# Optimization experiments

Hardware: AMD Instinct MI355X
Metric: run time of the kernel (lower is better)

Reference implementation:

```python
import jax, jax.numpy as jnp
import numpy as np

B, S, H = 1, 2048, 2048
E, I = 16, 1408
I_SHARED = 5632
TOP_K = 2


def setup_inputs() -> dict:
    key = jax.random.key(0)
    ks = jax.random.split(key, 8)
    scale = 0.02
    return {
        "hidden_states": jax.random.normal(ks[0], (B, S, H), dtype=jnp.float32),
        "router_w": jax.random.normal(ks[1], (H, E), dtype=jnp.float32) * scale,
        "expert_gate_up_w": jax.random.normal(ks[2], (E, H, 2 * I), dtype=jnp.float32) * scale,
        "expert_out_w": jax.random.normal(ks[3], (E, I, H), dtype=jnp.float32) * scale,
        "shared_ffw_gate_w": jax.random.normal(ks[4], (H, I_SHARED), dtype=jnp.float32) * scale,
        "shared_ffw_inter_w": jax.random.normal(ks[5], (H, I_SHARED), dtype=jnp.float32) * scale,
        "shared_ffw_out_w": jax.random.normal(ks[6], (I_SHARED, H), dtype=jnp.float32) * scale,
        "shared_gate_w": jax.random.normal(ks[7], (H, 1), dtype=jnp.float32) * scale,
        "top_k": TOP_K,
    }


def reference(hidden_states, router_w, expert_gate_up_w, expert_out_w,
              shared_ffw_gate_w, shared_ffw_inter_w, shared_ffw_out_w,
              shared_gate_w, top_k):
    b, s, h = hidden_states.shape
    e = router_w.shape[-1]
    x = hidden_states.reshape(-1, h)  # [T, H]

    # --- Router: softmax over experts, top-k, renormalize (norm_top_k_prob=True) ---
    router_logits = x @ router_w                        # [T, E]
    router_probs = jax.nn.softmax(router_logits, -1)
    top_p, top_i = jax.lax.top_k(router_probs, top_k)   # [T, K]
    top_p = top_p / jnp.sum(top_p, axis=-1, keepdims=True)
    # dense routing matrix [E, T] (matches one_hot-sum-transpose in source)
    one_hot = jax.nn.one_hot(top_i, e, dtype=top_p.dtype)  # [T, K, E]
    routing_full = jnp.sum(one_hot * top_p[..., None], axis=1).T  # [E, T]

    # --- Dense per-expert SwiGLU over ALL tokens (as in QwenMoeExperts) ---
    gate_up = jnp.einsum('th,ehm->etm', x, expert_gate_up_w)  # [E, T, 2I]
    gate, up = jnp.split(gate_up, 2, axis=-1)
    hidden = up * jax.nn.silu(gate)                           # [E, T, I]
    expert_out = jnp.einsum('eti,eih->eth', hidden, expert_out_w)  # [E, T, H]
    expert_contribution = jnp.einsum('eth,et->th', expert_out, routing_full)

    # --- Shared expert (SwiGLU MLP) with sigmoid gate ---
    sgate = jax.nn.silu(x @ shared_ffw_gate_w)
    sinter = x @ shared_ffw_inter_w
    shared_out = (sinter * sgate) @ shared_ffw_out_w          # [T, H]
    shared_out = shared_out * jax.nn.sigmoid(x @ shared_gate_w)

    out = (expert_contribution + shared_out).reshape(b, s, h)
    return out, router_logits
```

## Files before the change

kernel.cpp:

```cpp
#include <hip/hip_runtime.h>
#include <math.h>

typedef __attribute__((ext_vector_type(4))) float f32x4;
typedef __attribute__((ext_vector_type(4))) unsigned int u32x4;
typedef __attribute__((ext_vector_type(8))) unsigned short u16x8;
typedef __attribute__((ext_vector_type(8))) __bf16 bf16x8;
typedef unsigned short ushort_t;

#define H_DIM 2048
#define T_TOK 2048
#define NEXP 16
#define I_DIM 1408
#define I2_DIM 2816
#define IS_DIM 5632
#define MAXROWS 8192

static __device__ __forceinline__ unsigned short f2bf(float f){
  union { float f; unsigned u; } v; v.f = f;
  unsigned r = v.u + 0x7FFFu + ((v.u >> 16) & 1u);
  return (unsigned short)(r >> 16);
}
static __device__ __forceinline__ float bf2f(unsigned short h){
  union { unsigned u; float f; } v; v.u = ((unsigned)h) << 16;
  return v.f;
}
static __device__ __forceinline__ float silu_f(float x){ return x / (1.f + __expf(-x)); }

static __device__ __forceinline__ void gld16(const ushort_t* g, ushort_t* l){
  __builtin_amdgcn_global_load_lds(
      (const __attribute__((address_space(1))) unsigned int*)g,
      (__attribute__((address_space(3))) unsigned int*)l, 16, 0, 0);
}

static __device__ __forceinline__ bf16x8 dsr128(unsigned byte_off){
  u32x4 r;
  asm volatile("ds_read_b128 %0, %1" : "=v"(r) : "v"(byte_off));
  return __builtin_bit_cast(bf16x8, r);
}

__global__ void cast_bf16_k(const float* __restrict__ in, ushort_t* __restrict__ out){
  long i = ((long)blockIdx.x * 256 + threadIdx.x) * 8;
  f32x4 a = *(const f32x4*)&in[i];
  f32x4 b = *(const f32x4*)&in[i + 4];
  union { ushort_t s[8]; u32x4 v; } pk;
  #pragma unroll
  for (int j = 0; j < 4; j++){ pk.s[j] = f2bf(a[j]); pk.s[j+4] = f2bf(b[j]); }
  *(u32x4*)&out[i] = pk.v;
}

__global__ void transpose_cast_k(const float* __restrict__ in, ushort_t* __restrict__ out,
                                 int K, int N){
  long zo = (long)blockIdx.z * K * N;
  in += zo; out += zo;
  __shared__ float tl[64][65];
  int n0 = blockIdx.x * 64, k0 = blockIdx.y * 64;
  int tid = threadIdx.x;
  int lr = tid >> 2;
  int lv = (tid & 3) * 4;
  #pragma unroll
  for (int j = 0; j < 4; j++){
    int col = lv + j * 16;
    f32x4 v = *(const f32x4*)&in[(long)(k0 + lr) * N + n0 + col];
    tl[lr][col + 0] = v[0]; tl[lr][col + 1] = v[1];
    tl[lr][col + 2] = v[2]; tl[lr][col + 3] = v[3];
  }
  __syncthreads();
  int nl = tid >> 3;
  int kc = (tid & 7) * 8;
  #pragma unroll
  for (int it = 0; it < 2; it++){
    int n = nl + it * 32;
    union { ushort_t s[8]; u32x4 v; } pk;
    #pragma unroll
    for (int j = 0; j < 8; j++) pk.s[j] = f2bf(tl[kc + j][n]);
    *(u32x4*)&out[(long)(n0 + n) * K + k0 + kc] = pk.v;
  }
}

__global__ void router_k(const float* __restrict__ x, const float* __restrict__ rw,
                         const float* __restrict__ sgw, float* __restrict__ logits,
                         int* __restrict__ counts, int* __restrict__ lists,
                         float* __restrict__ probs, float* __restrict__ sgmul){
  int wid = threadIdx.x >> 6, lane = threadIdx.x & 63;
  int t = blockIdx.x * 4 + wid;
  const float* xr = x + (long)t * H_DIM;
  float acc[17];
  #pragma unroll
  for (int e = 0; e < 17; e++) acc[e] = 0.f;
  for (int h0 = lane * 4; h0 < H_DIM; h0 += 256){
    f32x4 xv = *(const f32x4*)&xr[h0];
    #pragma unroll
    for (int i = 0; i < 4; i++){
      float xs = xv[i];
      const float* wrow = rw + (long)(h0 + i) * NEXP;
      #pragma unroll
      for (int e = 0; e < 16; e++) acc[e] += xs * wrow[e];
      acc[16] += xs * sgw[h0 + i];
    }
  }
  #pragma unroll
  for (int e = 0; e < 17; e++)
    for (int off = 32; off >= 1; off >>= 1)
      acc[e] += __shfl_xor(acc[e], off);
  if (lane == 0){
    float* lo = logits + (long)t * NEXP;
    #pragma unroll
    for (int e = 0; e < 16; e++) lo[e] = acc[e];
    int e0 = 0;
    #pragma unroll
    for (int e = 1; e < 16; e++) if (acc[e] > acc[e0]) e0 = e;
    int e1 = (e0 == 0) ? 1 : 0;
    #pragma unroll
    for (int e = 0; e < 16; e++) if (e != e0 && acc[e] > acc[e1]) e1 = e;
    float d = acc[e1] - acc[e0];
    float ed = __expf(d);
    float p0 = 1.f / (1.f + ed);
    float p1 = ed / (1.f + ed);
    int pos0 = atomicAdd(&counts[e0], 1);
    lists[e0 * T_TOK + pos0] = t; probs[e0 * T_TOK + pos0] = p0;
    int pos1 = atomicAdd(&counts[e1], 1);
    lists[e1 * T_TOK + pos1] = t; probs[e1 * T_TOK + pos1] = p1;
    sgmul[t] = 1.f / (1.f + __expf(-acc[16]));
  }
}

__global__ void bases_k(const int* __restrict__ counts, int* __restrict__ bases){
  if (threadIdx.x == 0){
    int r = 0;
    for (int e = 0; e < NEXP; e++){ bases[e] = r; r += (counts[e] + 127) & ~127; }
  }
}

__global__ void swiglu_expert_k(const ushort_t* __restrict__ gu, ushort_t* __restrict__ hid){
  long qd = (long)blockIdx.x * 256 + threadIdx.x;
  long r = qd / (I_DIM / 8); int ic = (int)(qd % (I_DIM / 8)) * 8;
  const ushort_t* g = gu + r * I2_DIM + ic;
  u16x8 gv = *(const u16x8*)g;
  u16x8 uv = *(const u16x8*)(g + I_DIM);
  u16x8 ov;
  #pragma unroll
  for (int i = 0; i < 8; i++)
    ov[i] = f2bf(bf2f(uv[i]) * silu_f(bf2f(gv[i])));
  *(u16x8*)&hid[r * I_DIM + ic] = ov;
}

__global__ void swiglu_flat_k(ushort_t* __restrict__ sg, const ushort_t* __restrict__ si){
  long i = ((long)blockIdx.x * 256 + threadIdx.x) * 8;
  u16x8 g = *(const u16x8*)&sg[i];
  u16x8 s = *(const u16x8*)&si[i];
  u16x8 o;
  #pragma unroll
  for (int j = 0; j < 8; j++)
    o[j] = f2bf(bf2f(s[j]) * silu_f(bf2f(g[j])));
  *(u16x8*)&sg[i] = o;
}

template<int MODE>
static __device__ __forceinline__ void gemm3_body(
    const ushort_t* __restrict__ A, const ushort_t* __restrict__ Bt,
    const ushort_t* __restrict__ Bt2, ushort_t* __restrict__ Cb,
    int K, int lda, int ldbt, int ldc, int mb,
    const int* __restrict__ counts, const int* __restrict__ bases,
    const int* __restrict__ lists, const float* __restrict__ probs,
    const float* __restrict__ svec, float* __restrict__ outp, long bstride){
  int z = blockIdx.z;
  int cnt = T_TOK;
  const ushort_t* Ab = A;
  const ushort_t* Bb = Bt;
  long rbase = 0;
  if constexpr (MODE == 0){ if (z){ Bb = Bt2; Cb += (long)T_TOK * ldc; } }
  if constexpr (MODE == 1){ cnt = counts[z]; rbase = bases[z]; Bb += (long)z * bstride; }
  if constexpr (MODE == 2){ cnt = counts[z]; Ab += (long)bases[z] * lda; Bb += (long)z * bstride; }

  int kb = K / gridDim.y;
  int kbase = blockIdx.y * kb;
  Ab += kbase;
  Bb += kbase;

  int nwg = gridDim.x;
  int wgo = blockIdx.x;
  int q = nwg >> 3, r = nwg & 7;
  int xcd = wgo & 7, idx = wgo >> 3;
  int wg = (xcd < r ? xcd * (q + 1) : r * (q + 1) + (xcd - r) * q) + idx;
  int m0 = (wg % mb) * 128;
  if (m0 >= cnt) return;
  int n0 = (wg / mb) * 128;

  __shared__ ushort_t lds[3 * 8192];
  unsigned lbase = (unsigned)(size_t)(__attribute__((address_space(3))) ushort_t*)lds;

  int tid = threadIdx.x;
  int lane = tid & 63;
  int wv = tid >> 6;
  int wm = wv >> 1;
  int wn = wv & 1;

  int srow = lane >> 2;
  int sslot = ((lane & 3) ^ (srow & 3)) * 8;
  long aoff[2], boff[2];
  #pragma unroll
  for (int c = 0; c < 2; c++){
    int mr = wv * 32 + c * 16 + srow;
    int grow;
    if constexpr (MODE == 1){
      int j = m0 + mr; if (j >= cnt) j = cnt - 1;
      grow = lists[z * T_TOK + j];
    } else {
      grow = m0 + mr;
    }
    aoff[c] = (long)grow * lda + sslot;
    boff[c] = (long)(n0 + mr) * ldbt + sslot;
  }

  auto stage = [&](int t, int buf){
    long ko = (long)t * 32;
    ushort_t* dA = lds + buf * 8192 + wv * 32 * 32;
    ushort_t* dB = dA + 4096;
    gld16(Ab + aoff[0] + ko, dA);
    gld16(Ab + aoff[1] + ko, dA + 512);
    gld16(Bb + boff[0] + ko, dB);
    gld16(Bb + boff[1] + ko, dB + 512);
  };

  f32x4 zero = {0.f, 0.f, 0.f, 0.f};
  f32x4 acc[4][4];
  #pragma unroll
  for (int i = 0; i < 4; i++)
    #pragma unroll
    for (int j = 0; j < 4; j++) acc[i][j] = zero;

  int fr = lane & 15;
  int kg = lane >> 4;
  unsigned ps = (unsigned)((kg ^ (fr & 3)) << 4);
  unsigned aoffb = (unsigned)((wm * 64 + fr) * 64) + ps;
  unsigned boffb = 8192u + (unsigned)((wn * 64 + fr) * 64) + ps;

  int nt = kb >> 5;
  stage(0, 0);
  __builtin_amdgcn_sched_barrier(0);
  stage(1, 1);

  int rb = 0, sb = 2;
  for (int t = 0; t < nt; t++){
    if (t + 2 < nt) asm volatile("s_waitcnt vmcnt(4)" ::: "memory");
    else            asm volatile("s_waitcnt vmcnt(0)" ::: "memory");
    __builtin_amdgcn_s_barrier();
    __builtin_amdgcn_sched_barrier(0);
    unsigned bufb = lbase + (unsigned)rb * 16384u;
    bf16x8 af[4], bg[4];
    #pragma unroll
    for (int f = 0; f < 4; f++){
      af[f] = dsr128(bufb + aoffb + f * 1024u);
      bg[f] = dsr128(bufb + boffb + f * 1024u);
    }
    __builtin_amdgcn_sched_barrier(0);
    if (t + 2 < nt) stage(t + 2, sb);
    asm volatile("s_waitcnt lgkmcnt(0)" ::: "memory");
    __builtin_amdgcn_sched_barrier(0);
    __builtin_amdgcn_s_setprio(1);
    #pragma unroll
    for (int fm = 0; fm < 4; fm++)
      #pragma unroll
      for (int fn = 0; fn < 4; fn++)
        acc[fm][fn] = __builtin_amdgcn_mfma_f32_16x16x32_bf16(af[fm], bg[fn], acc[fm][fn], 0, 0, 0);
    __builtin_amdgcn_s_setprio(0);
    rb = (rb == 2) ? 0 : rb + 1;
    sb = (sb == 2) ? 0 : sb + 1;
  }

  int colb = n0 + wn * 64 + (lane & 15);
  int rowb = m0 + wm * 64 + (lane >> 4) * 4;
  #pragma unroll
  for (int fm = 0; fm < 4; fm++){
    #pragma unroll
    for (int fn = 0; fn < 4; fn++){
      f32x4 v = acc[fm][fn];
      int col = colb + fn * 16;
      #pragma unroll
      for (int rr = 0; rr < 4; rr++){
        int m = rowb + fm * 16 + rr;
        if constexpr (MODE == 0){
          Cb[(long)m * ldc + col] = f2bf(v[rr]);
        } else if constexpr (MODE == 1){
          if (m < cnt) Cb[(rbase + m) * (long)ldc + col] = f2bf(v[rr]);
        } else if constexpr (MODE == 2){
          if (m < cnt){
            int tok = lists[z * T_TOK + m];
            float pp = probs[z * T_TOK + m];
            atomicAdd(outp + (long)tok * ldc + col, pp * v[rr]);
          }
        } else {
          atomicAdd(outp + (long)m * ldc + col, svec[m] * v[rr]);
        }
      }
    }
  }
}

#define GEMM_ARGS const ushort_t* A, const ushort_t* Bt, const ushort_t* Bt2, ushort_t* Cb, \
    int K, int lda, int ldbt, int ldc, int mb, const int* counts, const int* bases, \
    const int* lists, const float* probs, const float* svec, float* outp, long bstride
#define GEMM_PASS A, Bt, Bt2, Cb, K, lda, ldbt, ldc, mb, counts, bases, lists, probs, svec, outp, bstride

__global__ __launch_bounds__(256) void g_shared_gi(GEMM_ARGS){ gemm3_body<0>(GEMM_PASS); }
__global__ __launch_bounds__(256) void g_shared_out(GEMM_ARGS){ gemm3_body<3>(GEMM_PASS); }
__global__ __launch_bounds__(256) void g_expert_gu(GEMM_ARGS){ gemm3_body<1>(GEMM_PASS); }
__global__ __launch_bounds__(256) void g_expert_out(GEMM_ARGS){ gemm3_body<2>(GEMM_PASS); }

extern "C" void kernel_launch(void* const* d_in, const int* in_sizes, int n_in,
                              void* d_out, int out_size, void* d_ws, size_t ws_size,
                              hipStream_t stream){
  const float* x    = (const float*)d_in[0];
  const float* rw   = (const float*)d_in[1];
  const float* wgu  = (const float*)d_in[2];
  const float* wout = (const float*)d_in[3];
  const float* wsg  = (const float*)d_in[4];
  const float* wsi  = (const float*)d_in[5];
  const float* wso  = (const float*)d_in[6];
  const float* sgw  = (const float*)d_in[7];

  float* out = (float*)d_out;
  float* logits = out + (size_t)T_TOK * H_DIM;

  char* w = (char*)d_ws;
  auto alloc = [&](size_t b){ char* p = w; w += (b + 255) & ~(size_t)255; return p; };
  ushort_t* xb     = (ushort_t*)alloc((size_t)T_TOK * H_DIM * 2);
  ushort_t* wgu_t  = (ushort_t*)alloc((size_t)NEXP * I2_DIM * H_DIM * 2);
  ushort_t* wout_t = (ushort_t*)alloc((size_t)NEXP * H_DIM * I_DIM * 2);
  ushort_t* wsg_t  = (ushort_t*)alloc((size_t)IS_DIM * H_DIM * 2);
  ushort_t* wsi_t  = (ushort_t*)alloc((size_t)IS_DIM * H_DIM * 2);
  ushort_t* wso_t  = (ushort_t*)alloc((size_t)H_DIM * IS_DIM * 2);
  ushort_t* sgr    = (ushort_t*)alloc((size_t)2 * T_TOK * IS_DIM * 2);
  ushort_t* sir    = sgr + (size_t)T_TOK * IS_DIM;
  ushort_t* gu     = (ushort_t*)alloc((size_t)MAXROWS * I2_DIM * 2);
  ushort_t* hid    = (ushort_t*)alloc((size_t)MAXROWS * I_DIM * 2);
  int*   counts = (int*)alloc(64);
  int*   bases  = (int*)alloc(64);
  int*   lists  = (int*)alloc((size_t)NEXP * T_TOK * 4);
  float* probs  = (float*)alloc((size_t)NEXP * T_TOK * 4);
  float* sgmul  = (float*)alloc((size_t)T_TOK * 4);

  hipMemsetAsync(counts, 0, 64, stream);
  hipMemsetAsync(out, 0, (size_t)T_TOK * H_DIM * sizeof(float), stream);

  cast_bf16_k<<<2048, 256, 0, stream>>>(x, xb);
  transpose_cast_k<<<dim3(I2_DIM/64, H_DIM/64, NEXP), 256, 0, stream>>>(wgu, wgu_t, H_DIM, I2_DIM);
  transpose_cast_k<<<dim3(H_DIM/64, I_DIM/64, NEXP), 256, 0, stream>>>(wout, wout_t, I_DIM, H_DIM);
  transpose_cast_k<<<dim3(IS_DIM/64, H_DIM/64, 1), 256, 0, stream>>>(wsg, wsg_t, H_DIM, IS_DIM);
  transpose_cast_k<<<dim3(IS_DIM/64, H_DIM/64, 1), 256, 0, stream>>>(wsi, wsi_t, H_DIM, IS_DIM);
  transpose_cast_k<<<dim3(H_DIM/64, IS_DIM/64, 1), 256, 0, stream>>>(wso, wso_t, IS_DIM, H_DIM);

  router_k<<<512, 256, 0, stream>>>(x, rw, sgw, logits, counts, lists, probs, sgmul);
  bases_k<<<1, 64, 0, stream>>>(counts, bases);

  g_shared_gi<<<dim3((T_TOK/128) * (IS_DIM/128), 1, 2), 256, 0, stream>>>(
      xb, wsg_t, wsi_t, sgr, H_DIM, H_DIM, H_DIM, IS_DIM, T_TOK/128,
      nullptr, nullptr, nullptr, nullptr, nullptr, nullptr, 0);
  swiglu_flat_k<<<(T_TOK * (IS_DIM/8)) / 256, 256, 0, stream>>>(sgr, sir);
  g_shared_out<<<dim3((T_TOK/128) * (H_DIM/128), 4, 1), 256, 0, stream>>>(
      sgr, wso_t, nullptr, nullptr, IS_DIM, IS_DIM, IS_DIM, H_DIM, T_TOK/128,
      nullptr, nullptr, nullptr, nullptr, sgmul, out, 0);

  g_expert_gu<<<dim3((T_TOK/128) * (I2_DIM/128), 1, NEXP), 256, 0, stream>>>(
      xb, wgu_t, nullptr, gu, H_DIM, H_DIM, H_DIM, I2_DIM, T_TOK/128,
      counts, bases, lists, probs, nullptr, nullptr, (long)I2_DIM * H_DIM);
  swiglu_expert_k<<<((long)MAXROWS * (I_DIM/8)) / 256, 256, 0, stream>>>(gu, hid);
  g_expert_out<<<dim3((T_TOK/128) * (H_DIM/128), 1, NEXP), 256, 0, stream>>>(
      hid, wout_t, nullptr, nullptr, I_DIM, I_DIM, I_DIM, H_DIM, T_TOK/128,
      counts, bases, lists, probs, nullptr, out, (long)I_DIM * H_DIM);

  (void)in_sizes; (void)n_in; (void)out_size; (void)ws_size;
}
```

Before: 798.9 us.

## Enlarge GEMM tiles to 256x256 with 512 threads and double buffering

Switches all four GEMM kernels from 128x128 tiles with 256 threads and a three-stage LDS ring to 256x256 tiles with 512 threads (eight waves, each computing a 128x64 sub-tile) and a two-buffer ping-pong. Expert row bases are now padded to multiples of 256 to match the new M tile. The goal is more data reuse per LDS load and fewer redundant global reads of weights and activations. The cost is a shallower prefetch, since each iteration waits with vmcnt(0), plus higher register pressure from 128 accumulator registers per lane. It also brings coarser wave quantization and more wasted padding rows on experts whose token counts are not multiples of 256.

```diff
diff --git a/kernel.cpp b/kernel.cpp
--- a/kernel.cpp
+++ b/kernel.cpp
@@ -36,6 +36,9 @@
   u32x4 r;
   asm volatile("ds_read_b128 %0, %1" : "=v"(r) : "v"(byte_off));
   return __builtin_bit_cast(bf16x8, r);
+}
+static __device__ __forceinline__ unsigned ldsaddr(const ushort_t* p){
+  return (unsigned)(size_t)(const __attribute__((address_space(3))) ushort_t*)p;
 }
 
 __global__ void cast_bf16_k(const float* __restrict__ in, ushort_t* __restrict__ out){
@@ -127,7 +130,7 @@
 __global__ void bases_k(const int* __restrict__ counts, int* __restrict__ bases){
   if (threadIdx.x == 0){
     int r = 0;
-    for (int e = 0; e < NEXP; e++){ bases[e] = r; r += (counts[e] + 127) & ~127; }
+    for (int e = 0; e < NEXP; e++){ bases[e] = r; r += (counts[e] + 255) & ~255; }
   }
 }
 
@@ -156,7 +159,7 @@
 }
 
 template<int MODE>
-static __device__ __forceinline__ void gemm3_body(
+static __device__ __forceinline__ void gemm4_body(
     const ushort_t* __restrict__ A, const ushort_t* __restrict__ Bt,
     const ushort_t* __restrict__ Bt2, ushort_t* __restrict__ Cb,
     int K, int lda, int ldbt, int ldc, int mb,
@@ -182,18 +185,17 @@
   int q = nwg >> 3, r = nwg & 7;
   int xcd = wgo & 7, idx = wgo >> 3;
   int wg = (xcd < r ? xcd * (q + 1) : r * (q + 1) + (xcd - r) * q) + idx;
-  int m0 = (wg % mb) * 128;
+  int m0 = (wg % mb) * 256;
   if (m0 >= cnt) return;
-  int n0 = (wg / mb) * 128;
-
-  __shared__ ushort_t lds[3 * 8192];
-  unsigned lbase = (unsigned)(size_t)(__attribute__((address_space(3))) ushort_t*)lds;
+  int n0 = (wg / mb) * 256;
+
+  __shared__ ushort_t A0[8192], B0[8192], A1[8192], B1[8192];
 
   int tid = threadIdx.x;
   int lane = tid & 63;
   int wv = tid >> 6;
-  int wm = wv >> 1;
-  int wn = wv & 1;
+  int wm = wv >> 2;
+  int wn = wv & 3;
 
   int srow = lane >> 2;
   int sslot = ((lane & 3) ^ (srow & 3)) * 8;
@@ -212,66 +214,66 @@
     boff[c] = (long)(n0 + mr) * ldbt + sslot;
   }
 
-  auto stage = [&](int t, int buf){
-    long ko = (long)t * 32;
-    ushort_t* dA = lds + buf * 8192 + wv * 32 * 32;
-    ushort_t* dB = dA + 4096;
-    gld16(Ab + aoff[0] + ko, dA);
-    gld16(Ab + aoff[1] + ko, dA + 512);
-    gld16(Bb + boff[0] + ko, dB);
-    gld16(Bb + boff[1] + ko, dB + 512);
+  auto stg = [&](long t, ushort_t* dA, ushort_t* dB){
+    long ko = t * 32;
+    ushort_t* wA = dA + wv * 1024;
+    ushort_t* wB = dB + wv * 1024;
+    gld16(Ab + aoff[0] + ko, wA);
+    gld16(Ab + aoff[1] + ko, wA + 512);
+    gld16(Bb + boff[0] + ko, wB);
+    gld16(Bb + boff[1] + ko, wB + 512);
   };
 
   f32x4 zero = {0.f, 0.f, 0.f, 0.f};
-  f32x4 acc[4][4];
-  #pragma unroll
-  for (int i = 0; i < 4; i++)
+  f32x4 acc[8][4];
+  #pragma unroll
+  for (int i = 0; i < 8; i++)
     #pragma unroll
     for (int j = 0; j < 4; j++) acc[i][j] = zero;
 
-  int fr = lane & 15;
-  int kg = lane >> 4;
-  unsigned ps = (unsigned)((kg ^ (fr & 3)) << 4);
-  unsigned aoffb = (unsigned)((wm * 64 + fr) * 64) + ps;
-  unsigned boffb = 8192u + (unsigned)((wn * 64 + fr) * 64) + ps;
+  unsigned ps = (unsigned)(((lane >> 4) ^ (lane & 3)) << 4);
+  unsigned aro = (unsigned)((wm * 128 + (lane & 15)) * 64) + ps;
+  unsigned bro = (unsigned)((wn * 64 + (lane & 15)) * 64) + ps;
+  unsigned a0b = ldsaddr(A0), b0b = ldsaddr(B0);
+  unsigned a1b = ldsaddr(A1), b1b = ldsaddr(B1);
 
   int nt = kb >> 5;
-  stage(0, 0);
-  __builtin_amdgcn_sched_barrier(0);
-  stage(1, 1);
-
-  int rb = 0, sb = 2;
-  for (int t = 0; t < nt; t++){
-    if (t + 2 < nt) asm volatile("s_waitcnt vmcnt(4)" ::: "memory");
-    else            asm volatile("s_waitcnt vmcnt(0)" ::: "memory");
-    __builtin_amdgcn_s_barrier();
-    __builtin_amdgcn_sched_barrier(0);
-    unsigned bufb = lbase + (unsigned)rb * 16384u;
-    bf16x8 af[4], bg[4];
-    #pragma unroll
-    for (int f = 0; f < 4; f++){
-      af[f] = dsr128(bufb + aoffb + f * 1024u);
-      bg[f] = dsr128(bufb + boffb + f * 1024u);
-    }
-    __builtin_amdgcn_sched_barrier(0);
-    if (t + 2 < nt) stage(t + 2, sb);
-    asm volatile("s_waitcnt lgkmcnt(0)" ::: "memory");
-    __builtin_amdgcn_sched_barrier(0);
-    __builtin_amdgcn_s_setprio(1);
-    #pragma unroll
-    for (int fm = 0; fm < 4; fm++)
-      #pragma unroll
-      for (int fn = 0; fn < 4; fn++)
-        acc[fm][fn] = __builtin_amdgcn_mfma_f32_16x16x32_bf16(af[fm], bg[fn], acc[fm][fn], 0, 0, 0);
-    __builtin_amdgcn_s_setprio(0);
-    rb = (rb == 2) ? 0 : rb + 1;
-    sb = (sb == 2) ? 0 : sb + 1;
-  }
+  stg(0, A0, B0);
+
+  #define BODY(T, CURA, CURB, NXA, NXB)                                          \
+  {                                                                              \
+    asm volatile("s_waitcnt vmcnt(0)" ::: "memory");                             \
+    __builtin_amdgcn_s_barrier();                                                \
+    __builtin_amdgcn_sched_barrier(0);                                           \
+    if ((T) + 1 < nt) stg((T) + 1, NXA, NXB);                                    \
+    __builtin_amdgcn_sched_barrier(0);                                           \
+    bf16x8 af[8], bg[4];                                                         \
+    _Pragma("unroll")                                                            \
+    for (int f = 0; f < 8; f++) af[f] = dsr128(CURA + aro + f * 1024u);          \
+    _Pragma("unroll")                                                            \
+    for (int f = 0; f < 4; f++) bg[f] = dsr128(CURB + bro + f * 1024u);          \
+    asm volatile("s_waitcnt lgkmcnt(0)" ::: "memory");                           \
+    __builtin_amdgcn_sched_barrier(0);                                           \
+    __builtin_amdgcn_s_setprio(1);                                               \
+    _Pragma("unroll")                                                            \
+    for (int fm = 0; fm < 8; fm++)                                               \
+      _Pragma("unroll")                                                          \
+      for (int fn = 0; fn < 4; fn++)                                             \
+        acc[fm][fn] = __builtin_amdgcn_mfma_f32_16x16x32_bf16(af[fm], bg[fn],    \
+                                                              acc[fm][fn], 0, 0, 0); \
+    __builtin_amdgcn_s_setprio(0);                                               \
+  }
+
+  for (int t = 0; t < nt; t += 2){
+    BODY(t,     a0b, b0b, A1, B1);
+    BODY(t + 1, a1b, b1b, A0, B0);
+  }
+  #undef BODY
 
   int colb = n0 + wn * 64 + (lane & 15);
-  int rowb = m0 + wm * 64 + (lane >> 4) * 4;
-  #pragma unroll
-  for (int fm = 0; fm < 4; fm++){
+  int rowb = m0 + wm * 128 + (lane >> 4) * 4;
+  #pragma unroll
+  for (int fm = 0; fm < 8; fm++){
     #pragma unroll
     for (int fn = 0; fn < 4; fn++){
       f32x4 v = acc[fm][fn];
@@ -302,10 +304,10 @@
     const int* lists, const float* probs, const float* svec, float* outp, long bstride
 #define GEMM_PASS A, Bt, Bt2, Cb, K, lda, ldbt, ldc, mb, counts, bases, lists, probs, svec, outp, bstride
 
-__global__ __launch_bounds__(256) void g_shared_gi(GEMM_ARGS){ gemm3_body<0>(GEMM_PASS); }
-__global__ __launch_bounds__(256) void g_shared_out(GEMM_ARGS){ gemm3_body<3>(GEMM_PASS); }
-__global__ __launch_bounds__(256) void g_expert_gu(GEMM_ARGS){ gemm3_body<1>(GEMM_PASS); }
-__global__ __launch_bounds__(256) void g_expert_out(GEMM_ARGS){ gemm3_body<2>(GEMM_PASS); }
+__global__ __launch_bounds__(512) void g_shared_gi(GEMM_ARGS){ gemm4_body<0>(GEMM_PASS); }
+__global__ __launch_bounds__(512) void g_shared_out(GEMM_ARGS){ gemm4_body<3>(GEMM_PASS); }
+__global__ __launch_bounds__(512) void g_expert_gu(GEMM_ARGS){ gemm4_body<1>(GEMM_PASS); }
+__global__ __launch_bounds__(512) void g_expert_out(GEMM_ARGS){ gemm4_body<2>(GEMM_PASS); }
 
 extern "C" void kernel_launch(void* const* d_in, const int* in_sizes, int n_in,
                               void* d_out, int out_size, void* d_ws, size_t ws_size,
@@ -353,20 +355,20 @@
   router_k<<<512, 256, 0, stream>>>(x, rw, sgw, logits, counts, lists, probs, sgmul);
   bases_k<<<1, 64, 0, stream>>>(counts, bases);
 
-  g_shared_gi<<<dim3((T_TOK/128) * (IS_DIM/128), 1, 2), 256, 0, stream>>>(
-      xb, wsg_t, wsi_t, sgr, H_DIM, H_DIM, H_DIM, IS_DIM, T_TOK/128,
+  g_shared_gi<<<dim3((T_TOK/256) * (IS_DIM/256), 1, 2), 512, 0, stream>>>(
+      xb, wsg_t, wsi_t, sgr, H_DIM, H_DIM, H_DIM, IS_DIM, T_TOK/256,
       nullptr, nullptr, nullptr, nullptr, nullptr, nullptr, 0);
   swiglu_flat_k<<<(T_TOK * (IS_DIM/8)) / 256, 256, 0, stream>>>(sgr, sir);
-  g_shared_out<<<dim3((T_TOK/128) * (H_DIM/128), 4, 1), 256, 0, stream>>>(
-      sgr, wso_t, nullptr, nullptr, IS_DIM, IS_DIM, IS_DIM, H_DIM, T_TOK/128,
+  g_shared_out<<<dim3((T_TOK/256) * (H_DIM/256), 4, 1), 512, 0, stream>>>(
+      sgr, wso_t, nullptr, nullptr, IS_DIM, IS_DIM, IS_DIM, H_DIM, T_TOK/256,
       nullptr, nullptr, nullptr, nullptr, sgmul, out, 0);
 
-  g_expert_gu<<<dim3((T_TOK/128) * (I2_DIM/128), 1, NEXP), 256, 0, stream>>>(
-      xb, wgu_t, nullptr, gu, H_DIM, H_DIM, H_DIM, I2_DIM, T_TOK/128,
+  g_expert_gu<<<dim3((T_TOK/256) * (I2_DIM/256), 1, NEXP), 512, 0, stream>>>(
+      xb, wgu_t, nullptr, gu, H_DIM, H_DIM, H_DIM, I2_DIM, T_TOK/256,
       counts, bases, lists, probs, nullptr, nullptr, (long)I2_DIM * H_DIM);
   swiglu_expert_k<<<((long)MAXROWS * (I_DIM/8)) / 256, 256, 0, stream>>>(gu, hid);
-  g_expert_out<<<dim3((T_TOK/128) * (H_DIM/128), 1, NEXP), 256, 0, stream>>>(
-      hid, wout_t, nullptr, nullptr, I_DIM, I_DIM, I_DIM, H_DIM, T_TOK/128,
+  g_expert_out<<<dim3((T_TOK/256) * (H_DIM/256), 1, NEXP), 512, 0, stream>>>(
+      hid, wout_t, nullptr, nullptr, I_DIM, I_DIM, I_DIM, H_DIM, T_TOK/256,
       counts, bases, lists, probs, nullptr, out, (long)I_DIM * H_DIM);
 
   (void)in_sizes; (void)n_in; (void)out_size; (void)ws_size;
```

Measured after the change: 928.0 us. 16.2% more time.

## Merge shared and routed expert GEMMs into combined up and down launches

Applied to the files above, without the earlier changes.

Replaces four separate GEMM launches with two: one up-projection kernel covering the shared gate/inter and per-expert gate_up GEMMs, and one down-projection kernel covering the shared output (split-K of 2) and per-expert output GEMMs. Work is dispatched by blockIdx.z, and the template MODE becomes a runtime emode argument. The intent is to fill the GPU better by letting small, uneven expert tiles run alongside the large shared tiles, and to remove launch gaps and tail effects between kernels. MAXROWS is also reduced so the expert SwiGLU pass covers fewer rows. In exchange, the runtime branches in the epilogue may cost registers, and many early-exiting blocks in the expert z-slices still take a launch slot.

```diff
diff --git a/kernel.cpp b/kernel.cpp
--- a/kernel.cpp
+++ b/kernel.cpp
@@ -13,7 +13,7 @@
 #define I_DIM 1408
 #define I2_DIM 2816
 #define IS_DIM 5632
-#define MAXROWS 8192
+#define MAXROWS 6144
 
 static __device__ __forceinline__ unsigned short f2bf(float f){
   union { float f; unsigned u; } v; v.f = f;
@@ -155,37 +155,14 @@
   *(u16x8*)&sg[i] = o;
 }
 
-template<int MODE>
-static __device__ __forceinline__ void gemm3_body(
-    const ushort_t* __restrict__ A, const ushort_t* __restrict__ Bt,
-    const ushort_t* __restrict__ Bt2, ushort_t* __restrict__ Cb,
-    int K, int lda, int ldbt, int ldc, int mb,
-    const int* __restrict__ counts, const int* __restrict__ bases,
-    const int* __restrict__ lists, const float* __restrict__ probs,
-    const float* __restrict__ svec, float* __restrict__ outp, long bstride){
-  int z = blockIdx.z;
-  int cnt = T_TOK;
-  const ushort_t* Ab = A;
-  const ushort_t* Bb = Bt;
-  long rbase = 0;
-  if constexpr (MODE == 0){ if (z){ Bb = Bt2; Cb += (long)T_TOK * ldc; } }
-  if constexpr (MODE == 1){ cnt = counts[z]; rbase = bases[z]; Bb += (long)z * bstride; }
-  if constexpr (MODE == 2){ cnt = counts[z]; Ab += (long)bases[z] * lda; Bb += (long)z * bstride; }
-
-  int kb = K / gridDim.y;
-  int kbase = blockIdx.y * kb;
-  Ab += kbase;
-  Bb += kbase;
-
-  int nwg = gridDim.x;
-  int wgo = blockIdx.x;
-  int q = nwg >> 3, r = nwg & 7;
-  int xcd = wgo & 7, idx = wgo >> 3;
-  int wg = (xcd < r ? xcd * (q + 1) : r * (q + 1) + (xcd - r) * q) + idx;
-  int m0 = (wg % mb) * 128;
-  if (m0 >= cnt) return;
-  int n0 = (wg / mb) * 128;
-
+static __device__ __forceinline__ void gemm_core(
+    const ushort_t* __restrict__ Ab, int lda,
+    const ushort_t* __restrict__ Bb, int ldbt,
+    int kb, int m0, int n0, int cnt,
+    const int* __restrict__ gather,
+    int emode, ushort_t* __restrict__ Cb, int ldc, long rbase,
+    const int* __restrict__ sclist, const float* __restrict__ scprob,
+    const float* __restrict__ svec, float* __restrict__ outp){
   __shared__ ushort_t lds[3 * 8192];
   unsigned lbase = (unsigned)(size_t)(__attribute__((address_space(3))) ushort_t*)lds;
 
@@ -202,9 +179,9 @@
   for (int c = 0; c < 2; c++){
     int mr = wv * 32 + c * 16 + srow;
     int grow;
-    if constexpr (MODE == 1){
+    if (gather){
       int j = m0 + mr; if (j >= cnt) j = cnt - 1;
-      grow = lists[z * T_TOK + j];
+      grow = gather[j];
     } else {
       grow = m0 + mr;
     }
@@ -214,7 +191,7 @@
 
   auto stage = [&](int t, int buf){
     long ko = (long)t * 32;
-    ushort_t* dA = lds + buf * 8192 + wv * 32 * 32;
+    ushort_t* dA = lds + buf * 8192 + wv * 1024;
     ushort_t* dB = dA + 4096;
     gld16(Ab + aoff[0] + ko, dA);
     gld16(Ab + aoff[1] + ko, dA + 512);
@@ -279,15 +256,14 @@
       #pragma unroll
       for (int rr = 0; rr < 4; rr++){
         int m = rowb + fm * 16 + rr;
-        if constexpr (MODE == 0){
+        if (emode == 0){
           Cb[(long)m * ldc + col] = f2bf(v[rr]);
-        } else if constexpr (MODE == 1){
+        } else if (emode == 1){
           if (m < cnt) Cb[(rbase + m) * (long)ldc + col] = f2bf(v[rr]);
-        } else if constexpr (MODE == 2){
+        } else if (emode == 2){
           if (m < cnt){
-            int tok = lists[z * T_TOK + m];
-            float pp = probs[z * T_TOK + m];
-            atomicAdd(outp + (long)tok * ldc + col, pp * v[rr]);
+            int tok = sclist[m];
+            atomicAdd(outp + (long)tok * ldc + col, scprob[m] * v[rr]);
           }
         } else {
           atomicAdd(outp + (long)m * ldc + col, svec[m] * v[rr]);
@@ -297,15 +273,63 @@
   }
 }
 
-#define GEMM_ARGS const ushort_t* A, const ushort_t* Bt, const ushort_t* Bt2, ushort_t* Cb, \
-    int K, int lda, int ldbt, int ldc, int mb, const int* counts, const int* bases, \
-    const int* lists, const float* probs, const float* svec, float* outp, long bstride
-#define GEMM_PASS A, Bt, Bt2, Cb, K, lda, ldbt, ldc, mb, counts, bases, lists, probs, svec, outp, bstride
-
-__global__ __launch_bounds__(256) void g_shared_gi(GEMM_ARGS){ gemm3_body<0>(GEMM_PASS); }
-__global__ __launch_bounds__(256) void g_shared_out(GEMM_ARGS){ gemm3_body<3>(GEMM_PASS); }
-__global__ __launch_bounds__(256) void g_expert_gu(GEMM_ARGS){ gemm3_body<1>(GEMM_PASS); }
-__global__ __launch_bounds__(256) void g_expert_out(GEMM_ARGS){ gemm3_body<2>(GEMM_PASS); }
+static __device__ __forceinline__ int swz_wg(){
+  int nwg = gridDim.x;
+  int wgo = blockIdx.x;
+  int q = nwg >> 3, r = nwg & 7;
+  int xcd = wgo & 7, idx = wgo >> 3;
+  return (xcd < r ? xcd * (q + 1) : r * (q + 1) + (xcd - r) * q) + idx;
+}
+
+__global__ __launch_bounds__(256) void g_up(
+    const ushort_t* xb, const ushort_t* wsg_t, const ushort_t* wsi_t,
+    const ushort_t* wgu_t, ushort_t* sgr, ushort_t* gu,
+    const int* counts, const int* bases, const int* lists){
+  int z = blockIdx.z;
+  int wg = swz_wg();
+  int mblk = wg & 15, nblk = wg >> 4;
+  int m0 = mblk * 128, n0 = nblk * 128;
+  if (z < 2){
+    gemm_core(xb, H_DIM, (z ? wsi_t : wsg_t), H_DIM, H_DIM, m0, n0, T_TOK,
+              nullptr, 0, sgr + (size_t)z * T_TOK * IS_DIM, IS_DIM, 0,
+              nullptr, nullptr, nullptr, nullptr);
+  } else {
+    int e = z - 2;
+    if (nblk >= I2_DIM / 128) return;
+    int cnt = counts[e];
+    if (m0 >= cnt) return;
+    gemm_core(xb, H_DIM, wgu_t + (size_t)e * I2_DIM * H_DIM, H_DIM, H_DIM,
+              m0, n0, cnt, lists + e * T_TOK,
+              1, gu, I2_DIM, bases[e],
+              nullptr, nullptr, nullptr, nullptr);
+  }
+}
+
+__global__ __launch_bounds__(256) void g_down(
+    const ushort_t* sgr, const ushort_t* hid,
+    const ushort_t* wso_t, const ushort_t* wout_t,
+    const int* counts, const int* bases, const int* lists,
+    const float* probs, const float* sgmul, float* out){
+  int z = blockIdx.z;
+  int wg = swz_wg();
+  int mblk = wg & 15, nblk = wg >> 4;
+  int m0 = mblk * 128, n0 = nblk * 128;
+  if (z < 2){
+    gemm_core(sgr + z * (IS_DIM / 2), IS_DIM, wso_t + z * (IS_DIM / 2), IS_DIM,
+              IS_DIM / 2, m0, n0, T_TOK, nullptr,
+              3, nullptr, H_DIM, 0,
+              nullptr, nullptr, sgmul, out);
+  } else {
+    int e = z - 2;
+    int cnt = counts[e];
+    if (m0 >= cnt) return;
+    gemm_core(hid + (size_t)bases[e] * I_DIM, I_DIM,
+              wout_t + (size_t)e * H_DIM * I_DIM, I_DIM,
+              I_DIM, m0, n0, cnt, nullptr,
+              2, nullptr, H_DIM, 0,
+              lists + e * T_TOK, probs + e * T_TOK, nullptr, out);
+  }
+}
 
 extern "C" void kernel_launch(void* const* d_in, const int* in_sizes, int n_in,
                               void* d_out, int out_size, void* d_ws, size_t ws_size,
@@ -353,21 +377,14 @@
   router_k<<<512, 256, 0, stream>>>(x, rw, sgw, logits, counts, lists, probs, sgmul);
   bases_k<<<1, 64, 0, stream>>>(counts, bases);
 
-  g_shared_gi<<<dim3((T_TOK/128) * (IS_DIM/128), 1, 2), 256, 0, stream>>>(
-      xb, wsg_t, wsi_t, sgr, H_DIM, H_DIM, H_DIM, IS_DIM, T_TOK/128,
-      nullptr, nullptr, nullptr, nullptr, nullptr, nullptr, 0);
+  g_up<<<dim3(16 * (IS_DIM/128), 1, 2 + NEXP), 256, 0, stream>>>(
+      xb, wsg_t, wsi_t, wgu_t, sgr, gu, counts, bases, lists);
+
   swiglu_flat_k<<<(T_TOK * (IS_DIM/8)) / 256, 256, 0, stream>>>(sgr, sir);
-  g_shared_out<<<dim3((T_TOK/128) * (H_DIM/128), 4, 1), 256, 0, stream>>>(
-      sgr, wso_t, nullptr, nullptr, IS_DIM, IS_DIM, IS_DIM, H_DIM, T_TOK/128,
-      nullptr, nullptr, nullptr, nullptr, sgmul, out, 0);
-
-  g_expert_gu<<<dim3((T_TOK/128) * (I2_DIM/128), 1, NEXP), 256, 0, stream>>>(
-      xb, wgu_t, nullptr, gu, H_DIM, H_DIM, H_DIM, I2_DIM, T_TOK/128,
-      counts, bases, lists, probs, nullptr, nullptr, (long)I2_DIM * H_DIM);
   swiglu_expert_k<<<((long)MAXROWS * (I_DIM/8)) / 256, 256, 0, stream>>>(gu, hid);
-  g_expert_out<<<dim3((T_TOK/128) * (H_DIM/128), 1, NEXP), 256, 0, stream>>>(
-      hid, wout_t, nullptr, nullptr, I_DIM, I_DIM, I_DIM, H_DIM, T_TOK/128,
-      counts, bases, lists, probs, nullptr, out, (long)I_DIM * H_DIM);
+
+  g_down<<<dim3(16 * (H_DIM/128), 1, 2 + NEXP), 256, 0, stream>>>(
+      sgr, hid, wso_t, wout_t, counts, bases, lists, probs, sgmul, out);
 
   (void)in_sizes; (void)n_in; (void)out_size; (void)ws_size;
 }
```

After: 829.7 us. 1.04x slower.
